# Kernel tuning notes

Hardware: AMD Instinct MI355X
Metric: run time of the kernel (lower is better)

## Reference

```python
import jax, jax.numpy as jnp
import numpy as np

B, S, D, H = 4, 2048, 1024, 16
HD = D // H


def setup_inputs() -> dict:
    key = jax.random.key(0)
    k1, k2, k3 = jax.random.split(key, 3)
    x = jax.random.normal(k1, (B, S, D), dtype=jnp.float32)
    # xavier-ish scaling for stable softmax
    W_attn = jax.random.normal(k2, (3 * D, D), dtype=jnp.float32) * (1.0 / np.sqrt(2 * D))
    b_attn = jnp.zeros((3 * D,), dtype=jnp.float32)
    W_out = jax.random.normal(k3, (D, D), dtype=jnp.float32) * (1.0 / np.sqrt(D))
    b_out = jnp.zeros((D,), dtype=jnp.float32)
    return {"x": x, "W_attn": W_attn, "b_attn": b_attn, "W_out": W_out, "b_out": b_out}


def reference(x, W_attn, b_attn, W_out, b_out):
    bs, seq, d = x.shape
    # fused QKV projection (torch Linear: y = x @ W.T + b)
    kqv = jnp.einsum("bsd,ed->bse", x, W_attn) + b_attn
    # NOTE: source splits as k, q, v (k first)
    k, q, v = jnp.split(kqv, 3, axis=2)
    # [b, s, h, hd] -> [b, h, s, hd]
    k = k.reshape(bs, seq, H, HD).transpose(0, 2, 1, 3)
    q = q.reshape(bs, seq, H, HD).transpose(0, 2, 1, 3)
    v = v.reshape(bs, seq, H, HD).transpose(0, 2, 1, 3)
    scale = 1.0 / np.sqrt(HD)
    scores = jnp.einsum("bhqd,bhkd->bhqk", q, k) * scale
    attn = jax.nn.softmax(scores, axis=-1)
    y = jnp.einsum("bhqk,bhkd->bhqd", attn, v)
    y = y.transpose(0, 2, 1, 3).reshape(bs, seq, d)
    out = jnp.einsum("bsd,ed->bse", y, W_out) + b_out
    return out
```

## Files before the change

kernel.cpp:

```cpp
#include <hip/hip_runtime.h>

typedef unsigned short u16;
typedef unsigned int u32;
typedef __attribute__((ext_vector_type(2))) u32 u32x2;
typedef __attribute__((ext_vector_type(4))) u32 u32x4;
typedef __attribute__((ext_vector_type(8))) short bf16x8;
typedef __attribute__((ext_vector_type(4))) float f32x4;

__device__ __forceinline__ u16 f2bf(float f) {
  u32 b = __float_as_uint(f);
  b += 0x7fffu + ((b >> 16) & 1u);
  return (u16)(b >> 16);
}

__device__ __forceinline__ u32 pk2bf(float a, float b) {
#if __has_builtin(__builtin_amdgcn_cvt_pk_bf16_f32)
  return __builtin_bit_cast(u32, __builtin_amdgcn_cvt_pk_bf16_f32(a, b));
#else
  return (u32)f2bf(a) | ((u32)f2bf(b) << 16);
#endif
}

__device__ __forceinline__ bf16x8 mk_ones8() {
  u32x4 t;
  t[0] = t[1] = t[2] = t[3] = 0x3F803F80u;
  return __builtin_bit_cast(bf16x8, t);
}

__device__ __forceinline__ float fexp2(float x) {
#if __has_builtin(__builtin_amdgcn_exp2f)
  return __builtin_amdgcn_exp2f(x);
#else
  return exp2f(x);
#endif
}

__device__ __forceinline__ void gload_lds16(const u16* g, u16* l) {
  __builtin_amdgcn_global_load_lds((const __attribute__((address_space(1))) void*)g,
                                   (__attribute__((address_space(3))) void*)l, 16, 0, 0);
}

__global__ __launch_bounds__(256) void cvt_all(const float* __restrict__ x,
                                               const float* __restrict__ wa,
                                               const float* __restrict__ wo,
                                               u16* __restrict__ xb,
                                               u16* __restrict__ wab,
                                               u16* __restrict__ wob) {
  int blk = blockIdx.x;
  const float* in;
  u16* out;
  long base;
  if (blk < 4096) {
    in = x; out = xb; base = blk;
  } else if (blk < 5632) {
    in = wa; out = wab; base = blk - 4096;
  } else {
    in = wo; out = wob; base = blk - 5632;
  }
  long i = (base * 256 + threadIdx.x) * 8;
  u32 u[8];
#pragma unroll
  for (int j = 0; j < 8; j++) {
    u32 b = __float_as_uint(in[i + j]);
    u[j] = (b + 0x7fffu + ((b >> 16) & 1u)) >> 16;
  }
  u32x4 o;
  o[0] = u[0] | (u[1] << 16);
  o[1] = u[2] | (u[3] << 16);
  o[2] = u[4] | (u[5] << 16);
  o[3] = u[6] | (u[7] << 16);
  *(u32x4*)(out + i) = o;
}

__device__ __forceinline__ void gemm_core_128(const u16* __restrict__ A,
                                              const u16* __restrict__ B, int K,
                                              int m0, int n0, u16* As, u16* Bs,
                                              f32x4 acc[4][4]) {
  int t = threadIdx.x;
  int lane = t & 63, w = t >> 6;
  int quad = lane >> 4, l16 = lane & 15;
  int wm = (w >> 1) * 64, wn = (w & 1) * 64;
  int lr = lane >> 3, lc = lane & 7;
  int cg = lc ^ lr;
  int swz = l16 & 7;
  for (int k0 = 0; k0 < K; k0 += 64) {
#pragma unroll
    for (int i = 0; i < 4; i++) {
      int r0 = i * 32 + w * 8;
      gload_lds16(&A[(long)(m0 + r0 + lr) * K + k0 + cg * 8], &As[r0 * 64]);
      gload_lds16(&B[(long)(n0 + r0 + lr) * K + k0 + cg * 8], &Bs[r0 * 64]);
    }
    __syncthreads();
#pragma unroll
    for (int ks = 0; ks < 2; ks++) {
      bf16x8 a[4], b[4];
#pragma unroll
      for (int tm = 0; tm < 4; tm++)
        a[tm] = *(const bf16x8*)&As[(wm + tm * 16 + l16) * 64 + ((ks * 4 + quad) ^ swz) * 8];
#pragma unroll
      for (int tn = 0; tn < 4; tn++)
        b[tn] = *(const bf16x8*)&Bs[(wn + tn * 16 + l16) * 64 + ((ks * 4 + quad) ^ swz) * 8];
#pragma unroll
      for (int tm = 0; tm < 4; tm++)
#pragma unroll
        for (int tn = 0; tn < 4; tn++)
          acc[tm][tn] = __builtin_amdgcn_mfma_f32_16x16x32_bf16(a[tm], b[tn],
                                                                acc[tm][tn], 0, 0, 0);
    }
    __syncthreads();
  }
}

#define QSCALE 0.1803368801f
__global__ __launch_bounds__(256) void gemm_qkv(const u16* __restrict__ A,
                                                const u16* __restrict__ B,
                                                const float* __restrict__ bias,
                                                u16* __restrict__ Kg,
                                                u16* __restrict__ Qg,
                                                u16* __restrict__ Vg) {
  __shared__ __align__(16) u16 As[128 * 64];
  __shared__ __align__(16) u16 Bs[128 * 64];
  const int K = 1024;
  int m0 = blockIdx.y * 128, n0 = blockIdx.x * 128;
  f32x4 acc[4][4];
#pragma unroll
  for (int i = 0; i < 4; i++)
#pragma unroll
    for (int j = 0; j < 4; j++) acc[i][j] = (f32x4)0.0f;
  gemm_core_128(A, B, K, m0, n0, As, Bs, acc);

  int t = threadIdx.x, lane = t & 63, w = t >> 6;
  int quad = lane >> 4, l16 = lane & 15;
  int wm = (w >> 1) * 64, wn = (w & 1) * 64;
  int which = m0 >> 10;
#pragma unroll
  for (int tm = 0; tm < 4; tm++) {
    int m = m0 + wm + tm * 16 + quad * 4;
    int h = (m >> 6) & 15, d0 = m & 63;
    f32x4 b4 = *(const f32x4*)&bias[m];
#pragma unroll
    for (int tn = 0; tn < 4; tn++) {
      int n = n0 + wn + tn * 16 + l16;
      int b = n >> 11, s = n & 2047;
      long bh = (long)b * 16 + h;
      if (which == 0) {
        u32x2 pk;
        pk[0] = pk2bf(acc[tm][tn][0] + b4[0], acc[tm][tn][1] + b4[1]);
        pk[1] = pk2bf(acc[tm][tn][2] + b4[2], acc[tm][tn][3] + b4[3]);
        *(u32x2*)&Kg[(bh * 2048 + s) * 64 + d0] = pk;
      } else if (which == 1) {
        u32x2 pk;
        pk[0] = pk2bf((acc[tm][tn][0] + b4[0]) * QSCALE,
                      (acc[tm][tn][1] + b4[1]) * QSCALE);
        pk[1] = pk2bf((acc[tm][tn][2] + b4[2]) * QSCALE,
                      (acc[tm][tn][3] + b4[3]) * QSCALE);
        *(u32x2*)&Qg[(bh * 2048 + s) * 64 + d0] = pk;
      } else {
#pragma unroll
        for (int r = 0; r < 4; r++)
          Vg[(bh * 64 + d0 + r) * 2048 + s] = f2bf(acc[tm][tn][r] + b4[r]);
      }
    }
  }
}

__global__ __launch_bounds__(256) void gemm_out(const u16* __restrict__ A,
                                                const u16* __restrict__ B,
                                                const float* __restrict__ bias,
                                                float* __restrict__ out) {
  __shared__ __align__(16) u16 As[128 * 64];
  __shared__ __align__(16) u16 Bs[128 * 64];
  const int K = 1024;
  int m0 = blockIdx.y * 128, n0 = blockIdx.x * 128;
  f32x4 acc[4][4];
#pragma unroll
  for (int i = 0; i < 4; i++)
#pragma unroll
    for (int j = 0; j < 4; j++) acc[i][j] = (f32x4)0.0f;
  gemm_core_128(A, B, K, m0, n0, As, Bs, acc);

  int t = threadIdx.x, lane = t & 63, w = t >> 6;
  int quad = lane >> 4, l16 = lane & 15;
  int wm = (w >> 1) * 64, wn = (w & 1) * 64;
#pragma unroll
  for (int tm = 0; tm < 4; tm++) {
    int m = m0 + wm + tm * 16 + quad * 4;
    f32x4 b4 = *(const f32x4*)&bias[m];
#pragma unroll
    for (int tn = 0; tn < 4; tn++) {
      int n = n0 + wn + tn * 16 + l16;
      f32x4 o = acc[tm][tn] + b4;
      *(f32x4*)&out[(long)n * 1024 + m] = o;
    }
  }
}

#define SYNC                                       \
  __builtin_amdgcn_sched_barrier(0);               \
  asm volatile("s_waitcnt vmcnt(0)" ::: "memory"); \
  __builtin_amdgcn_s_barrier();                    \
  __builtin_amdgcn_sched_barrier(0)

#define STAGE_KV(tt, bb)                                      \
  do {                                                        \
    gload_lds16(Kst + (long)(tt)*4096, &Ks[bb][w * 8 * 64]);  \
    gload_lds16(Vst + (tt)*64, &Vs[bb][w * 8 * 64]);          \
  } while (0)

#define COMPUTE(bb)                                                            \
  do {                                                                         \
    bf16x8 pf_[2][2];                                                          \
    _Pragma("unroll") for (int tq = 0; tq < 2; tq++) {                         \
      f32x4 s_[4];                                                             \
      __builtin_amdgcn_s_setprio(1);                                           \
      _Pragma("unroll") for (int tn = 0; tn < 4; tn++) {                       \
        bf16x8 kf0 = *(const bf16x8*)(kL0 + (bb)*4096 + tn * 1024);            \
        bf16x8 kf1 = *(const bf16x8*)(kL1 + (bb)*4096 + tn * 1024);            \
        s_[tn] = __builtin_amdgcn_mfma_f32_16x16x32_bf16(kf0, qf[tq][0], Z,    \
                                                         0, 0, 0);             \
        s_[tn] = __builtin_amdgcn_mfma_f32_16x16x32_bf16(kf1, qf[tq][1],       \
                                                         s_[tn], 0, 0, 0);     \
      }                                                                        \
      __builtin_amdgcn_s_setprio(0);                                           \
      _Pragma("unroll") for (int tn = 0; tn < 4; tn++) {                       \
        float e0 = fexp2(s_[tn][0]);                                           \
        float e1 = fexp2(s_[tn][1]);                                           \
        float e2 = fexp2(s_[tn][2]);                                           \
        float e3 = fexp2(s_[tn][3]);                                           \
        u32x2 pk;                                                              \
        pk[0] = pk2bf(e0, e1);                                                 \
        pk[1] = pk2bf(e2, e3);                                                 \
        *(u32x2*)(pW + tq * 1024 + woff[tn]) = pk;                             \
      }                                                                        \
    }                                                                          \
    _Pragma("unroll") for (int ks = 0; ks < 2; ks++)                           \
        _Pragma("unroll") for (int tq = 0; tq < 2; tq++) {                     \
      u32x2 lo = *(const u32x2*)(pR + tq * 1024 + prlo[ks]);                   \
      u32x2 hi = *(const u32x2*)(pR + tq * 1024 + prhi[ks]);                   \
      u32x4 cc;                                                                \
      cc[0] = lo[0];                                                           \
      cc[1] = lo[1];                                                           \
      cc[2] = hi[0];                                                           \
      cc[3] = hi[1];                                                           \
      pf_[tq][ks] = __builtin_bit_cast(bf16x8, cc);                            \
    }                                                                          \
    __builtin_amdgcn_s_setprio(1);                                             \
    _Pragma("unroll") for (int ks = 0; ks < 2; ks++) {                         \
      acc_sum[0] = __builtin_amdgcn_mfma_f32_16x16x32_bf16(ONES, pf_[0][ks],   \
                                                           acc_sum[0], 0, 0, 0); \
      acc_sum[1] = __builtin_amdgcn_mfma_f32_16x16x32_bf16(ONES, pf_[1][ks],   \
                                                           acc_sum[1], 0, 0, 0); \
      _Pragma("unroll") for (int dt = 0; dt < 4; dt++) {                       \
        bf16x8 vf = *(const bf16x8*)(vL[ks] + (bb)*4096 + dt * 1024);          \
        acc[dt][0] = __builtin_amdgcn_mfma_f32_16x16x32_bf16(vf, pf_[0][ks],   \
                                                             acc[dt][0], 0, 0, 0); \
        acc[dt][1] = __builtin_amdgcn_mfma_f32_16x16x32_bf16(vf, pf_[1][ks],   \
                                                             acc[dt][1], 0, 0, 0); \
      }                                                                        \
    }                                                                          \
    __builtin_amdgcn_s_setprio(0);                                             \
  } while (0)

__global__ __launch_bounds__(512, 4) void attn_kernel(const u16* __restrict__ Qg,
                                                      const u16* __restrict__ Kg,
                                                      const u16* __restrict__ Vg,
                                                      u16* __restrict__ Y) {
  __shared__ __align__(16) u16 Ks[2][64 * 64];
  __shared__ __align__(16) u16 Vs[2][64 * 64];
  __shared__ __align__(16) u16 Ps[8 * 32 * 64];
  int t = threadIdx.x, lane = t & 63, w = t >> 6;
  int quad = lane >> 4, l16 = lane & 15;
  int bh = blockIdx.y;
  int q0 = blockIdx.x * 256 + w * 32;
  int lr = lane >> 3, lc = lane & 7, cg = lc ^ lr;
  int swz = l16 & 7;
  u16* Pw = Ps + w * 2048;

  bf16x8 qf[2][2];
#pragma unroll
  for (int tq = 0; tq < 2; tq++) {
    const u16* qp = Qg + ((long)bh * 2048 + q0 + tq * 16 + l16) * 64;
    qf[tq][0] = *(const bf16x8*)(qp + quad * 8);
    qf[tq][1] = *(const bf16x8*)(qp + 32 + quad * 8);
  }

  const f32x4 Z = {0.0f, 0.0f, 0.0f, 0.0f};
  const bf16x8 ONES = mk_ones8();

  f32x4 acc[4][2];
  f32x4 acc_sum[2];
#pragma unroll
  for (int dt = 0; dt < 4; dt++)
#pragma unroll
    for (int tq = 0; tq < 2; tq++) acc[dt][tq] = (f32x4)0.0f;
  acc_sum[0] = (f32x4)0.0f;
  acc_sum[1] = (f32x4)0.0f;

  const u16* kL0 = &Ks[0][l16 * 64 + (quad ^ swz) * 8];
  const u16* kL1 = &Ks[0][l16 * 64 + ((4 + quad) ^ swz) * 8];
  const u16* vL[2] = {&Vs[0][l16 * 64 + (quad ^ swz) * 8],
                      &Vs[0][l16 * 64 + ((4 + quad) ^ swz) * 8]};
  u16* pW = Pw + l16 * 64;
  const u16* pR = Pw + l16 * 64;
  int woff[4], prlo[2], prhi[2];
#pragma unroll
  for (int tn = 0; tn < 4; tn++) woff[tn] = ((tn * 4 + quad) ^ l16) * 4;
#pragma unroll
  for (int ks = 0; ks < 2; ks++) {
    prlo[ks] = ((ks * 8 + quad * 2) ^ l16) * 4;
    prhi[ks] = ((ks * 8 + quad * 2 + 1) ^ l16) * 4;
  }

  const u16* Kst = Kg + ((long)bh * 2048 + w * 8 + lr) * 64 + cg * 8;
  const u16* Vst = Vg + ((long)(bh * 64 + w * 8 + lr)) * 2048 + cg * 8;

  STAGE_KV(0, 0);
  for (int tt = 0; tt < 30; tt += 2) {
    SYNC;
    STAGE_KV(tt + 1, 1);
    COMPUTE(0);
    SYNC;
    STAGE_KV(tt + 2, 0);
    COMPUTE(1);
  }
  SYNC;
  STAGE_KV(31, 1);
  COMPUTE(0);
  SYNC;
  COMPUTE(1);

  int b = bh >> 4, h = bh & 15;
#pragma unroll
  for (int tq = 0; tq < 2; tq++) {
    float inv = 1.0f / acc_sum[tq][0];
    long row = (long)b * 2048 + q0 + tq * 16 + l16;
#pragma unroll
    for (int dt = 0; dt < 4; dt++) {
      u32x2 pk;
      pk[0] = pk2bf(acc[dt][tq][0] * inv, acc[dt][tq][1] * inv);
      pk[1] = pk2bf(acc[dt][tq][2] * inv, acc[dt][tq][3] * inv);
      *(u32x2*)&Y[row * 1024 + h * 64 + dt * 16 + quad * 4] = pk;
    }
  }
}

extern "C" void kernel_launch(void* const* d_in, const int* in_sizes, int n_in,
                              void* d_out, int out_size, void* d_ws, size_t ws_size,
                              hipStream_t stream) {
  const float* x = (const float*)d_in[0];
  const float* W_attn = (const float*)d_in[1];
  const float* b_attn = (const float*)d_in[2];
  const float* W_out = (const float*)d_in[3];
  const float* b_out = (const float*)d_in[4];
  float* out = (float*)d_out;

  char* ws = (char*)d_ws;
  u16* xb = (u16*)ws;
  u16* Wab = (u16*)(ws + 16777216);
  u16* Wob = (u16*)(ws + 16777216 + 6291456);
  u16* Kg = (u16*)(ws + 25165824);
  u16* Qg = Kg + 8388608;
  u16* Vg = Qg + 8388608;
  u16* Yb = xb;

  cvt_all<<<6144, 256, 0, stream>>>(x, W_attn, W_out, xb, Wab, Wob);

  gemm_qkv<<<dim3(64, 24), 256, 0, stream>>>(Wab, xb, b_attn, Kg, Qg, Vg);
  attn_kernel<<<dim3(8, 64), 512, 0, stream>>>(Qg, Kg, Vg, Yb);
  gemm_out<<<dim3(64, 8), 256, 0, stream>>>(Wob, Yb, b_out, out);
}
```

Baseline: 278.3 us.

## Rewrite QKV GEMM as 256x256 tile with 4-stage LDS pipeline

Replaces the 128x128 single-buffer QKV GEMM with a 256x256 tile per 512-thread block that uses a 4-stage ring of 32-wide K slices in LDS. Async global-to-LDS loads are issued three stages ahead, with explicit vmcnt waits and raw barriers, and MFMA blocks are interleaved with the staging loads under raised wave priority. The aim is to hide global memory latency and cut the per-iteration barrier overhead while raising arithmetic intensity per block. In exchange the grid shrinks to 384 blocks, the kernel uses more LDS and registers, and correctness depends on the hand-tuned wait counts.

```diff
diff --git a/kernel.cpp b/kernel.cpp
--- a/kernel.cpp
+++ b/kernel.cpp
@@ -33,6 +33,10 @@
 #else
   return exp2f(x);
 #endif
+}
+
+__device__ __forceinline__ f32x4 mfma32(bf16x8 a, bf16x8 b, f32x4 c) {
+  return __builtin_amdgcn_mfma_f32_16x16x32_bf16(a, b, c, 0, 0, 0);
 }
 
 __device__ __forceinline__ void gload_lds16(const u16* g, u16* l) {
@@ -72,6 +76,146 @@
   *(u32x4*)(out + i) = o;
 }
 
+__device__ __forceinline__ void gemm256_core(const u16* __restrict__ A,
+                                             const u16* __restrict__ B,
+                                             int m0, int n0, u16* As, u16* Bs,
+                                             f32x4 acc[8][4]) {
+  const int K = 1024;
+  int t = threadIdx.x, lane = t & 63, w = t >> 6;
+  int quad = lane >> 4, l16 = lane & 15;
+  int wm = w >> 2, wn = w & 3;
+  int lrow = lane >> 2;
+  int lchunk = (lane & 3) ^ ((lane >> 3) & 3);
+  const u16* Ag0 = A + (long)(m0 + w * 32 + lrow) * K + lchunk * 8;
+  const u16* Ag1 = A + (long)(m0 + w * 32 + 16 + lrow) * K + lchunk * 8;
+  const u16* Bg0 = B + (long)(n0 + w * 32 + lrow) * K + lchunk * 8;
+  const u16* Bg1 = B + (long)(n0 + w * 32 + 16 + lrow) * K + lchunk * 8;
+  u16* Asw0 = As + (w * 32) * 32;
+  u16* Asw1 = As + (w * 32 + 16) * 32;
+  u16* Bsw0 = Bs + (w * 32) * 32;
+  u16* Bsw1 = Bs + (w * 32 + 16) * 32;
+  int rk = (quad ^ ((l16 >> 1) & 3)) * 8;
+  const u16* aR = As + (wm * 128 + l16) * 32 + rk;
+  const u16* bR = Bs + (wn * 64 + l16) * 32 + rk;
+
+#define STG_A9(kk, ss)                                \
+  do {                                                \
+    gload_lds16(Ag0 + (kk), Asw0 + (ss) * 8192);      \
+    gload_lds16(Ag1 + (kk), Asw1 + (ss) * 8192);      \
+  } while (0)
+#define STG_B9(kk, ss)                                \
+  do {                                                \
+    gload_lds16(Bg0 + (kk), Bsw0 + (ss) * 8192);      \
+    gload_lds16(Bg1 + (kk), Bsw1 + (ss) * 8192);      \
+  } while (0)
+
+  STG_A9(0, 0);
+  STG_B9(0, 0);
+  STG_A9(32, 1);
+  STG_B9(32, 1);
+  STG_A9(64, 2);
+  STG_B9(64, 2);
+
+  for (int hb = 0; hb < 32; hb += 4) {
+#pragma unroll
+    for (int j = 0; j < 4; j++) {
+      const int ss = j;
+      const int sst = (j + 3) & 3;
+      int kst = ((hb + j + 3) & 31) * 32;
+      __builtin_amdgcn_sched_barrier(0);
+      asm volatile("s_waitcnt vmcnt(8)" ::: "memory");
+      __builtin_amdgcn_s_barrier();
+      __builtin_amdgcn_sched_barrier(0);
+      STG_A9(kst, sst);
+      bf16x8 af[8], bfr[4];
+#pragma unroll
+      for (int mf = 0; mf < 4; mf++)
+        af[mf] = *(const bf16x8*)(aR + ss * 8192 + mf * 512);
+#pragma unroll
+      for (int nf = 0; nf < 4; nf++)
+        bfr[nf] = *(const bf16x8*)(bR + ss * 8192 + nf * 512);
+      asm volatile("s_waitcnt lgkmcnt(0)" ::: "memory");
+      __builtin_amdgcn_sched_barrier(0);
+      __builtin_amdgcn_s_setprio(1);
+#pragma unroll
+      for (int mf = 0; mf < 4; mf++)
+#pragma unroll
+        for (int nf = 0; nf < 4; nf++)
+          acc[mf][nf] = mfma32(af[mf], bfr[nf], acc[mf][nf]);
+      __builtin_amdgcn_s_setprio(0);
+      __builtin_amdgcn_sched_barrier(0);
+      STG_B9(kst, sst);
+#pragma unroll
+      for (int mf = 4; mf < 8; mf++)
+        af[mf] = *(const bf16x8*)(aR + ss * 8192 + mf * 512);
+      asm volatile("s_waitcnt lgkmcnt(0)" ::: "memory");
+      __builtin_amdgcn_sched_barrier(0);
+      __builtin_amdgcn_s_setprio(1);
+#pragma unroll
+      for (int mf = 4; mf < 8; mf++)
+#pragma unroll
+        for (int nf = 0; nf < 4; nf++)
+          acc[mf][nf] = mfma32(af[mf], bfr[nf], acc[mf][nf]);
+      __builtin_amdgcn_s_setprio(0);
+      __builtin_amdgcn_sched_barrier(0);
+    }
+  }
+#undef STG_A9
+#undef STG_B9
+}
+
+#define QSCALE 0.1803368801f
+__global__ __launch_bounds__(512, 2) void gemm_qkv(const u16* __restrict__ A,
+                                                   const u16* __restrict__ B,
+                                                   const float* __restrict__ bias,
+                                                   u16* __restrict__ Kg,
+                                                   u16* __restrict__ Qg,
+                                                   u16* __restrict__ Vg) {
+  __shared__ __align__(16) u16 As[4][256 * 32];
+  __shared__ __align__(16) u16 Bs[4][256 * 32];
+  int m0 = blockIdx.y * 256, n0 = blockIdx.x * 256;
+  f32x4 acc[8][4];
+#pragma unroll
+  for (int i = 0; i < 8; i++)
+#pragma unroll
+    for (int j = 0; j < 4; j++) acc[i][j] = (f32x4)0.0f;
+  gemm256_core(A, B, m0, n0, &As[0][0], &Bs[0][0], acc);
+
+  int t = threadIdx.x, lane = t & 63, w = t >> 6;
+  int quad = lane >> 4, l16 = lane & 15;
+  int wm = w >> 2, wn = w & 3;
+  int which = m0 >> 10;
+#pragma unroll
+  for (int mf = 0; mf < 8; mf++) {
+    int m = m0 + wm * 128 + mf * 16 + quad * 4;
+    int h = (m >> 6) & 15, d0 = m & 63;
+    f32x4 b4 = *(const f32x4*)&bias[m];
+#pragma unroll
+    for (int nf = 0; nf < 4; nf++) {
+      int n = n0 + wn * 64 + nf * 16 + l16;
+      int b = n >> 11, s = n & 2047;
+      long bh = (long)b * 16 + h;
+      if (which == 0) {
+        u32x2 pk;
+        pk[0] = pk2bf(acc[mf][nf][0] + b4[0], acc[mf][nf][1] + b4[1]);
+        pk[1] = pk2bf(acc[mf][nf][2] + b4[2], acc[mf][nf][3] + b4[3]);
+        *(u32x2*)&Kg[(bh * 2048 + s) * 64 + d0] = pk;
+      } else if (which == 1) {
+        u32x2 pk;
+        pk[0] = pk2bf((acc[mf][nf][0] + b4[0]) * QSCALE,
+                      (acc[mf][nf][1] + b4[1]) * QSCALE);
+        pk[1] = pk2bf((acc[mf][nf][2] + b4[2]) * QSCALE,
+                      (acc[mf][nf][3] + b4[3]) * QSCALE);
+        *(u32x2*)&Qg[(bh * 2048 + s) * 64 + d0] = pk;
+      } else {
+#pragma unroll
+        for (int r = 0; r < 4; r++)
+          Vg[(bh * 64 + d0 + r) * 2048 + s] = f2bf(acc[mf][nf][r] + b4[r]);
+      }
+    }
+  }
+}
+
 __device__ __forceinline__ void gemm_core_128(const u16* __restrict__ A,
                                               const u16* __restrict__ B, int K,
                                               int m0, int n0, u16* As, u16* Bs,
@@ -108,59 +252,6 @@
                                                                 acc[tm][tn], 0, 0, 0);
     }
     __syncthreads();
-  }
-}
-
-#define QSCALE 0.1803368801f
-__global__ __launch_bounds__(256) void gemm_qkv(const u16* __restrict__ A,
-                                                const u16* __restrict__ B,
-                                                const float* __restrict__ bias,
-                                                u16* __restrict__ Kg,
-                                                u16* __restrict__ Qg,
-                                                u16* __restrict__ Vg) {
-  __shared__ __align__(16) u16 As[128 * 64];
-  __shared__ __align__(16) u16 Bs[128 * 64];
-  const int K = 1024;
-  int m0 = blockIdx.y * 128, n0 = blockIdx.x * 128;
-  f32x4 acc[4][4];
-#pragma unroll
-  for (int i = 0; i < 4; i++)
-#pragma unroll
-    for (int j = 0; j < 4; j++) acc[i][j] = (f32x4)0.0f;
-  gemm_core_128(A, B, K, m0, n0, As, Bs, acc);
-
-  int t = threadIdx.x, lane = t & 63, w = t >> 6;
-  int quad = lane >> 4, l16 = lane & 15;
-  int wm = (w >> 1) * 64, wn = (w & 1) * 64;
-  int which = m0 >> 10;
-#pragma unroll
-  for (int tm = 0; tm < 4; tm++) {
-    int m = m0 + wm + tm * 16 + quad * 4;
-    int h = (m >> 6) & 15, d0 = m & 63;
-    f32x4 b4 = *(const f32x4*)&bias[m];
-#pragma unroll
-    for (int tn = 0; tn < 4; tn++) {
-      int n = n0 + wn + tn * 16 + l16;
-      int b = n >> 11, s = n & 2047;
-      long bh = (long)b * 16 + h;
-      if (which == 0) {
-        u32x2 pk;
-        pk[0] = pk2bf(acc[tm][tn][0] + b4[0], acc[tm][tn][1] + b4[1]);
-        pk[1] = pk2bf(acc[tm][tn][2] + b4[2], acc[tm][tn][3] + b4[3]);
-        *(u32x2*)&Kg[(bh * 2048 + s) * 64 + d0] = pk;
-      } else if (which == 1) {
-        u32x2 pk;
-        pk[0] = pk2bf((acc[tm][tn][0] + b4[0]) * QSCALE,
-                      (acc[tm][tn][1] + b4[1]) * QSCALE);
-        pk[1] = pk2bf((acc[tm][tn][2] + b4[2]) * QSCALE,
-                      (acc[tm][tn][3] + b4[3]) * QSCALE);
-        *(u32x2*)&Qg[(bh * 2048 + s) * 64 + d0] = pk;
-      } else {
-#pragma unroll
-        for (int r = 0; r < 4; r++)
-          Vg[(bh * 64 + d0 + r) * 2048 + s] = f2bf(acc[tm][tn][r] + b4[r]);
-      }
-    }
   }
 }
 
@@ -365,7 +456,7 @@
 
   cvt_all<<<6144, 256, 0, stream>>>(x, W_attn, W_out, xb, Wab, Wob);
 
-  gemm_qkv<<<dim3(64, 24), 256, 0, stream>>>(Wab, xb, b_attn, Kg, Qg, Vg);
+  gemm_qkv<<<dim3(32, 12), 512, 0, stream>>>(Wab, xb, b_attn, Kg, Qg, Vg);
   attn_kernel<<<dim3(8, 64), 512, 0, stream>>>(Qg, Kg, Vg, Yb);
   gemm_out<<<dim3(64, 8), 256, 0, stream>>>(Wob, Yb, b_out, out);
 }
```

Result: no change. 282.5 us (+1.5%).

## Pipeline GEMM core with a 3-stage LDS ring and one barrier per step

Applied to the files above, without the earlier changes.

Replaces the synchronous GEMM main loop, which loads a 64-wide K tile and then computes with two barriers per step, by a 3-stage ring of 32-wide K tiles in LDS. Global-to-LDS loads for two steps ahead are issued before each step's MFMAs. Each step uses a single vmcnt-guarded barrier, a new XOR swizzle and setprio around the MFMA block. The aim is to hide global load latency behind compute, at the cost of more LDS per block (48KB) and a fixed K=1024 schedule.

```diff
diff --git a/kernel.cpp b/kernel.cpp
--- a/kernel.cpp
+++ b/kernel.cpp
@@ -33,6 +33,10 @@
 #else
   return exp2f(x);
 #endif
+}
+
+__device__ __forceinline__ f32x4 mfma32(bf16x8 a, bf16x8 b, f32x4 c) {
+  return __builtin_amdgcn_mfma_f32_16x16x32_bf16(a, b, c, 0, 0, 0);
 }
 
 __device__ __forceinline__ void gload_lds16(const u16* g, u16* l) {
@@ -72,62 +76,98 @@
   *(u32x4*)(out + i) = o;
 }
 
-__device__ __forceinline__ void gemm_core_128(const u16* __restrict__ A,
-                                              const u16* __restrict__ B, int K,
-                                              int m0, int n0, u16* As, u16* Bs,
-                                              f32x4 acc[4][4]) {
-  int t = threadIdx.x;
-  int lane = t & 63, w = t >> 6;
+__device__ __forceinline__ void gemm_core_r3(const u16* __restrict__ A,
+                                             const u16* __restrict__ B,
+                                             int m0, int n0, u16* lds,
+                                             f32x4 acc[4][4]) {
+  const int K = 1024;
+  int t = threadIdx.x, lane = t & 63, w = t >> 6;
   int quad = lane >> 4, l16 = lane & 15;
   int wm = (w >> 1) * 64, wn = (w & 1) * 64;
-  int lr = lane >> 3, lc = lane & 7;
-  int cg = lc ^ lr;
-  int swz = l16 & 7;
-  for (int k0 = 0; k0 < K; k0 += 64) {
-#pragma unroll
-    for (int i = 0; i < 4; i++) {
-      int r0 = i * 32 + w * 8;
-      gload_lds16(&A[(long)(m0 + r0 + lr) * K + k0 + cg * 8], &As[r0 * 64]);
-      gload_lds16(&B[(long)(n0 + r0 + lr) * K + k0 + cg * 8], &Bs[r0 * 64]);
-    }
-    __syncthreads();
-#pragma unroll
-    for (int ks = 0; ks < 2; ks++) {
-      bf16x8 a[4], b[4];
-#pragma unroll
-      for (int tm = 0; tm < 4; tm++)
-        a[tm] = *(const bf16x8*)&As[(wm + tm * 16 + l16) * 64 + ((ks * 4 + quad) ^ swz) * 8];
-#pragma unroll
-      for (int tn = 0; tn < 4; tn++)
-        b[tn] = *(const bf16x8*)&Bs[(wn + tn * 16 + l16) * 64 + ((ks * 4 + quad) ^ swz) * 8];
-#pragma unroll
-      for (int tm = 0; tm < 4; tm++)
-#pragma unroll
-        for (int tn = 0; tn < 4; tn++)
-          acc[tm][tn] = __builtin_amdgcn_mfma_f32_16x16x32_bf16(a[tm], b[tn],
-                                                                acc[tm][tn], 0, 0, 0);
-    }
-    __syncthreads();
-  }
+  int lrow = lane >> 2;
+  int lchunk = (lane & 3) ^ ((lane >> 3) & 3);
+  const u16* Ag0 = A + (long)(m0 + w * 16 + lrow) * K + lchunk * 8;
+  const u16* Ag1 = A + (long)(m0 + 64 + w * 16 + lrow) * K + lchunk * 8;
+  const u16* Bg0 = B + (long)(n0 + w * 16 + lrow) * K + lchunk * 8;
+  const u16* Bg1 = B + (long)(n0 + 64 + w * 16 + lrow) * K + lchunk * 8;
+  u16* Ad0 = lds + (w * 16) * 32;
+  u16* Ad1 = lds + (64 + w * 16) * 32;
+  u16* Bd0 = lds + 4096 + (w * 16) * 32;
+  u16* Bd1 = lds + 4096 + (64 + w * 16) * 32;
+  int rk = (quad ^ ((l16 >> 1) & 3)) * 8;
+  const u16* aR = lds + (wm + l16) * 32 + rk;
+  const u16* bR = lds + 4096 + (wn + l16) * 32 + rk;
+
+#define STG_R3(kk, ss)                            \
+  do {                                            \
+    gload_lds16(Ag0 + (kk), Ad0 + (ss) * 8192);   \
+    gload_lds16(Ag1 + (kk), Ad1 + (ss) * 8192);   \
+    gload_lds16(Bg0 + (kk), Bd0 + (ss) * 8192);   \
+    gload_lds16(Bg1 + (kk), Bd1 + (ss) * 8192);   \
+  } while (0)
+
+#define BOUND_R3                                     \
+  __builtin_amdgcn_sched_barrier(0);                 \
+  asm volatile("s_waitcnt vmcnt(4)" ::: "memory");   \
+  __builtin_amdgcn_s_barrier();                      \
+  __builtin_amdgcn_sched_barrier(0)
+
+#define CMP_R3(ss)                                                   \
+  do {                                                               \
+    bf16x8 a_[4], b_[4];                                             \
+    _Pragma("unroll") for (int tm = 0; tm < 4; tm++)                 \
+        a_[tm] = *(const bf16x8*)(aR + (ss) * 8192 + tm * 512);      \
+    _Pragma("unroll") for (int tn = 0; tn < 4; tn++)                 \
+        b_[tn] = *(const bf16x8*)(bR + (ss) * 8192 + tn * 512);      \
+    asm volatile("s_waitcnt lgkmcnt(0)" ::: "memory");               \
+    __builtin_amdgcn_sched_barrier(0);                               \
+    __builtin_amdgcn_s_setprio(1);                                   \
+    _Pragma("unroll") for (int tm = 0; tm < 4; tm++)                 \
+        _Pragma("unroll") for (int tn = 0; tn < 4; tn++)             \
+            acc[tm][tn] = mfma32(a_[tm], b_[tn], acc[tm][tn]);       \
+    __builtin_amdgcn_s_setprio(0);                                   \
+    __builtin_amdgcn_sched_barrier(0);                               \
+  } while (0)
+
+  STG_R3(0, 0);
+  STG_R3(32, 1);
+  for (int hb = 0; hb < 30; hb += 3) {
+    BOUND_R3;
+    STG_R3(((hb + 2) & 31) * 32, 2);
+    CMP_R3(0);
+    BOUND_R3;
+    STG_R3(((hb + 3) & 31) * 32, 0);
+    CMP_R3(1);
+    BOUND_R3;
+    STG_R3(((hb + 4) & 31) * 32, 1);
+    CMP_R3(2);
+  }
+  BOUND_R3;
+  STG_R3(0, 2);
+  CMP_R3(0);
+  BOUND_R3;
+  CMP_R3(1);
+  asm volatile("s_waitcnt vmcnt(0)" ::: "memory");
+#undef STG_R3
+#undef BOUND_R3
+#undef CMP_R3
 }
 
 #define QSCALE 0.1803368801f
-__global__ __launch_bounds__(256) void gemm_qkv(const u16* __restrict__ A,
-                                                const u16* __restrict__ B,
-                                                const float* __restrict__ bias,
-                                                u16* __restrict__ Kg,
-                                                u16* __restrict__ Qg,
-                                                u16* __restrict__ Vg) {
-  __shared__ __align__(16) u16 As[128 * 64];
-  __shared__ __align__(16) u16 Bs[128 * 64];
-  const int K = 1024;
+__global__ __launch_bounds__(256, 3) void gemm_qkv(const u16* __restrict__ A,
+                                                   const u16* __restrict__ B,
+                                                   const float* __restrict__ bias,
+                                                   u16* __restrict__ Kg,
+                                                   u16* __restrict__ Qg,
+                                                   u16* __restrict__ Vg) {
+  __shared__ __align__(16) u16 ring[3 * 8192];
   int m0 = blockIdx.y * 128, n0 = blockIdx.x * 128;
   f32x4 acc[4][4];
 #pragma unroll
   for (int i = 0; i < 4; i++)
 #pragma unroll
     for (int j = 0; j < 4; j++) acc[i][j] = (f32x4)0.0f;
-  gemm_core_128(A, B, K, m0, n0, As, Bs, acc);
+  gemm_core_r3(A, B, m0, n0, ring, acc);
 
   int t = threadIdx.x, lane = t & 63, w = t >> 6;
   int quad = lane >> 4, l16 = lane & 15;
@@ -164,20 +204,18 @@
   }
 }
 
-__global__ __launch_bounds__(256) void gemm_out(const u16* __restrict__ A,
-                                                const u16* __restrict__ B,
-                                                const float* __restrict__ bias,
-                                                float* __restrict__ out) {
-  __shared__ __align__(16) u16 As[128 * 64];
-  __shared__ __align__(16) u16 Bs[128 * 64];
-  const int K = 1024;
+__global__ __launch_bounds__(256, 3) void gemm_out(const u16* __restrict__ A,
+                                                   const u16* __restrict__ B,
+                                                   const float* __restrict__ bias,
+                                                   float* __restrict__ out) {
+  __shared__ __align__(16) u16 ring[3 * 8192];
   int m0 = blockIdx.y * 128, n0 = blockIdx.x * 128;
   f32x4 acc[4][4];
 #pragma unroll
   for (int i = 0; i < 4; i++)
 #pragma unroll
     for (int j = 0; j < 4; j++) acc[i][j] = (f32x4)0.0f;
-  gemm_core_128(A, B, K, m0, n0, As, Bs, acc);
+  gemm_core_r3(A, B, m0, n0, ring, acc);
 
   int t = threadIdx.x, lane = t & 63, w = t >> 6;
   int quad = lane >> 4, l16 = lane & 15;
```

After: 274.1 us. Within noise of the previous version (-1.5%).
